# Kernel optimization log

Measured on AMD Instinct MI355X. Metric: run time of the kernel, lower is better.

## Reference

```python
import jax, jax.numpy as jnp
import numpy as np

N_LAYERS = 10
N_BLOCKS = 2
N_FILTERS = 2
N_CHANNELS = 1
KERNEL = 2
DIL_BASE = 2
N_RES = N_BLOCKS * N_LAYERS


def conv1d(x, w, b, dilation, pad):
    # x: [B, Cin, L], w: [Cout, Cin, K], b: [Cout]
    y = jax.lax.conv_general_dilated(
        x, w, window_strides=(1,), padding=[(pad, pad)],
        rhs_dilation=(dilation,), dimension_numbers=("NCH", "OIH", "NCH"))
    return y + b[None, :, None]


def setup_inputs() -> dict:
    key = jax.random.key(0)
    ks = jax.random.split(key, 9)
    B, C, L = 64, N_CHANNELS, 32768
    f = N_FILTERS
    s_in = 1.0 / np.sqrt(C * 1)          # conv_in fan-in (k=1)
    s_res = 1.0 / np.sqrt(f * KERNEL)    # residual conv fan-in
    s_out = 1.0 / np.sqrt(f * 1)         # conv_out fan-in (k=1)
    return {
        "x": jax.random.normal(ks[0], (B, C, L), dtype=jnp.float32),
        "conv_in_w": jax.random.normal(ks[1], (f, C, 1), dtype=jnp.float32) * s_in,
        "conv_in_b": jax.random.normal(ks[2], (f,), dtype=jnp.float32) * s_in,
        "wd": jax.random.normal(ks[3], (N_RES, f, f, KERNEL), dtype=jnp.float32) * s_res,
        "bd": jax.random.normal(ks[4], (N_RES, f), dtype=jnp.float32) * s_res,
        "wg": jax.random.normal(ks[5], (N_RES, f, f, KERNEL), dtype=jnp.float32) * s_res,
        "bg": jax.random.normal(ks[6], (N_RES, f), dtype=jnp.float32) * s_res,
        "conv_out_w": jax.random.normal(ks[7], (C, f, 1), dtype=jnp.float32) * s_out,
        "conv_out_b": jax.random.normal(ks[8], (C,), dtype=jnp.float32) * s_out,
    }


def reference(x, conv_in_w, conv_in_b, wd, bd, wg, bg, conv_out_w, conv_out_b):
    h = conv1d(x, conv_in_w, conv_in_b, 1, 0)  # [B, F, L]
    skips = []
    for i in range(N_RES):
        d = DIL_BASE ** (i // N_LAYERS)        # dilation constant within a block
        pad = (KERNEL - 1) * d // 2            # torch padding (padding arg is 0)
        cd = conv1d(h, wd[i], bd[i], d, pad)
        cg = conv1d(h, wg[i], bg[i], d, pad)
        g = cd * jax.nn.sigmoid(cg)            # gated activation (tanh unused in source)
        skips.append(g)
        # res = x[:, :, -g.size(2):] + g
        h = h[:, :, h.shape[2] - g.shape[2]:] + g
    # Faithful to torch: len(s) is the BATCH dim, so skips are truncated to time len B
    max_len = min(s.shape[0] for s in skips)
    s = skips[0][:, :, :max_len]
    for si in skips[1:]:
        s = s + si[:, :, :max_len]
    return conv1d(jax.nn.relu(s), conv_out_w, conv_out_b, 1, 0)
```

## Files before the change

kernel.cpp:

```cpp
#include <hip/hip_runtime.h>
#include <math.h>


#define N_RES   20
#define N_L1    10
#define W       96
#define OUT_L   64

__global__ __launch_bounds__(128) void wavenet_window_kernel(
    const float* __restrict__ x,
    const float* __restrict__ cin_w,
    const float* __restrict__ cin_b,
    const float* __restrict__ wd,
    const float* __restrict__ bd,
    const float* __restrict__ wg,
    const float* __restrict__ bg,
    const float* __restrict__ cout_w,
    const float* __restrict__ cout_b,
    float* __restrict__ out,
    int L)
{
    __shared__ float hbuf[2][2][W];
    __shared__ float skip[2][OUT_L];

    const int b   = blockIdx.x;
    const int tid = threadIdx.x;
    const float* xb = x + (size_t)b * (size_t)L;

    for (int idx = tid; idx < 2 * W; idx += blockDim.x) {
        const int f = idx / W, l = idx % W;
        hbuf[0][f][l] = cin_w[f] * xb[l] + cin_b[f];
    }
    for (int idx = tid; idx < 2 * OUT_L; idx += blockDim.x) {
        skip[idx / OUT_L][idx % OUT_L] = 0.0f;
    }
    __syncthreads();

    int cur = 0;
    int valid = W;
    for (int i = 0; i < N_RES; ++i) {
        const int d = (i < N_L1) ? 1 : 2;
        const float* wdi = wd + i * 8;
        const float* wgi = wg + i * 8;
        const float bd0 = bd[i * 2 + 0], bd1 = bd[i * 2 + 1];
        const float bg0 = bg[i * 2 + 0], bg1 = bg[i * 2 + 1];
        const int nout = valid - 1;

        for (int idx = tid; idx < 2 * W; idx += blockDim.x) {
            const int f = idx / W, l = idx % W;
            if (l < nout) {
                const int t0 = l - (d - 1);
                const float a0 = (t0 >= 0) ? hbuf[cur][0][t0] : 0.0f;
                const float a1 = (t0 >= 0) ? hbuf[cur][1][t0] : 0.0f;
                const float c0 = hbuf[cur][0][l + 1];
                const float c1 = hbuf[cur][1][l + 1];

                const float bdv = (f == 0) ? bd0 : bd1;
                const float bgv = (f == 0) ? bg0 : bg1;
                const float cd = wdi[f*4 + 0] * a0 + wdi[f*4 + 1] * c0
                               + wdi[f*4 + 2] * a1 + wdi[f*4 + 3] * c1 + bdv;
                const float cg = wgi[f*4 + 0] * a0 + wgi[f*4 + 1] * c0
                               + wgi[f*4 + 2] * a1 + wgi[f*4 + 3] * c1 + bgv;

                const float g = cd * (1.0f / (1.0f + expf(-cg)));
                const float hres = (d == 1) ? hbuf[cur][f][l + 1] : hbuf[cur][f][l];
                hbuf[1 - cur][f][l] = hres + g;
                if (l < OUT_L) skip[f][l] += g;
            }
        }
        __syncthreads();
        cur = 1 - cur;
        valid = nout;
    }

    const float w0 = cout_w[0], w1 = cout_w[1], bo = cout_b[0];
    for (int l = tid; l < OUT_L; l += blockDim.x) {
        const float s0 = fmaxf(skip[0][l], 0.0f);
        const float s1 = fmaxf(skip[1][l], 0.0f);
        out[(size_t)b * OUT_L + l] = w0 * s0 + w1 * s1 + bo;
    }
}

extern "C" void kernel_launch(void* const* d_in, const int* in_sizes, int n_in,
                              void* d_out, int out_size, void* d_ws, size_t ws_size,
                              hipStream_t stream) {
    const float* x      = (const float*)d_in[0];
    const float* cin_w  = (const float*)d_in[1];
    const float* cin_b  = (const float*)d_in[2];
    const float* wd     = (const float*)d_in[3];
    const float* bd     = (const float*)d_in[4];
    const float* wg     = (const float*)d_in[5];
    const float* bg     = (const float*)d_in[6];
    const float* cout_w = (const float*)d_in[7];
    const float* cout_b = (const float*)d_in[8];
    float* out = (float*)d_out;

    const int B = 64;
    const int L = in_sizes[0] / B;

    wavenet_window_kernel<<<B, 128, 0, stream>>>(
        x, cin_w, cin_b, wd, bd, wg, bg, cout_w, cout_b, out, L);
}
```

Measured before the change: 84.08 us.

## Remap to one wavefront per window computing both filters per lane

Shrinks each block to a single 64-lane wavefront, so each lane computes both output filters for its time position. This shares the four input loads from shared memory and removes the per-element filter branch. The 16 weights per layer are loaded once into scalars instead of being indexed per element, and expf is replaced with the faster, less precise __expf. With only one wavefront, __syncthreads becomes cheap, but the block has half as many threads to hide latency.

```diff
diff --git a/kernel.cpp b/kernel.cpp
--- a/kernel.cpp
+++ b/kernel.cpp
@@ -7,7 +7,7 @@
 #define W       96
 #define OUT_L   64
 
-__global__ __launch_bounds__(128) void wavenet_window_kernel(
+__global__ __launch_bounds__(64) void wavenet_window_kernel(
     const float* __restrict__ x,
     const float* __restrict__ cin_w,
     const float* __restrict__ cin_b,
@@ -23,16 +23,23 @@
     __shared__ float hbuf[2][2][W];
     __shared__ float skip[2][OUT_L];
 
-    const int b   = blockIdx.x;
-    const int tid = threadIdx.x;
+    const int b    = blockIdx.x;
+    const int lane = threadIdx.x;
     const float* xb = x + (size_t)b * (size_t)L;
 
-    for (int idx = tid; idx < 2 * W; idx += blockDim.x) {
-        const int f = idx / W, l = idx % W;
-        hbuf[0][f][l] = cin_w[f] * xb[l] + cin_b[f];
-    }
-    for (int idx = tid; idx < 2 * OUT_L; idx += blockDim.x) {
-        skip[idx / OUT_L][idx % OUT_L] = 0.0f;
+    {
+        const float cw0 = cin_w[0], cw1 = cin_w[1];
+        const float cb0 = cin_b[0], cb1 = cin_b[1];
+        const float xv = xb[lane];
+        hbuf[0][0][lane] = cw0 * xv + cb0;
+        hbuf[0][1][lane] = cw1 * xv + cb1;
+        if (lane < W - 64) {
+            const float xv2 = xb[lane + 64];
+            hbuf[0][0][lane + 64] = cw0 * xv2 + cb0;
+            hbuf[0][1][lane + 64] = cw1 * xv2 + cb1;
+        }
+        skip[0][lane] = 0.0f;
+        skip[1][lane] = 0.0f;
     }
     __syncthreads();
 
@@ -42,12 +49,17 @@
         const int d = (i < N_L1) ? 1 : 2;
         const float* wdi = wd + i * 8;
         const float* wgi = wg + i * 8;
+        const float wd00 = wdi[0], wd01 = wdi[1], wd02 = wdi[2], wd03 = wdi[3];
+        const float wd10 = wdi[4], wd11 = wdi[5], wd12 = wdi[6], wd13 = wdi[7];
+        const float wg00 = wgi[0], wg01 = wgi[1], wg02 = wgi[2], wg03 = wgi[3];
+        const float wg10 = wgi[4], wg11 = wgi[5], wg12 = wgi[6], wg13 = wgi[7];
         const float bd0 = bd[i * 2 + 0], bd1 = bd[i * 2 + 1];
         const float bg0 = bg[i * 2 + 0], bg1 = bg[i * 2 + 1];
         const int nout = valid - 1;
+        const int nxt  = 1 - cur;
 
-        for (int idx = tid; idx < 2 * W; idx += blockDim.x) {
-            const int f = idx / W, l = idx % W;
+        for (int l0 = 0; l0 < nout; l0 += 64) {
+            const int l = l0 + lane;
             if (l < nout) {
                 const int t0 = l - (d - 1);
                 const float a0 = (t0 >= 0) ? hbuf[cur][0][t0] : 0.0f;
@@ -55,30 +67,33 @@
                 const float c0 = hbuf[cur][0][l + 1];
                 const float c1 = hbuf[cur][1][l + 1];
 
-                const float bdv = (f == 0) ? bd0 : bd1;
-                const float bgv = (f == 0) ? bg0 : bg1;
-                const float cd = wdi[f*4 + 0] * a0 + wdi[f*4 + 1] * c0
-                               + wdi[f*4 + 2] * a1 + wdi[f*4 + 3] * c1 + bdv;
-                const float cg = wgi[f*4 + 0] * a0 + wgi[f*4 + 1] * c0
-                               + wgi[f*4 + 2] * a1 + wgi[f*4 + 3] * c1 + bgv;
+                const float cd_0 = wd00*a0 + wd01*c0 + wd02*a1 + wd03*c1 + bd0;
+                const float cg_0 = wg00*a0 + wg01*c0 + wg02*a1 + wg03*c1 + bg0;
+                const float cd_1 = wd10*a0 + wd11*c0 + wd12*a1 + wd13*c1 + bd1;
+                const float cg_1 = wg10*a0 + wg11*c0 + wg12*a1 + wg13*c1 + bg1;
 
-                const float g = cd * (1.0f / (1.0f + expf(-cg)));
-                const float hres = (d == 1) ? hbuf[cur][f][l + 1] : hbuf[cur][f][l];
-                hbuf[1 - cur][f][l] = hres + g;
-                if (l < OUT_L) skip[f][l] += g;
+                const float g0 = cd_0 * (1.0f / (1.0f + __expf(-cg_0)));
+                const float g1 = cd_1 * (1.0f / (1.0f + __expf(-cg_1)));
+
+                const float hr0 = (d == 1) ? hbuf[cur][0][l + 1] : hbuf[cur][0][l];
+                const float hr1 = (d == 1) ? hbuf[cur][1][l + 1] : hbuf[cur][1][l];
+                hbuf[nxt][0][l] = hr0 + g0;
+                hbuf[nxt][1][l] = hr1 + g1;
+                if (l < OUT_L) {
+                    skip[0][l] += g0;
+                    skip[1][l] += g1;
+                }
             }
         }
         __syncthreads();
-        cur = 1 - cur;
+        cur = nxt;
         valid = nout;
     }
 
     const float w0 = cout_w[0], w1 = cout_w[1], bo = cout_b[0];
-    for (int l = tid; l < OUT_L; l += blockDim.x) {
-        const float s0 = fmaxf(skip[0][l], 0.0f);
-        const float s1 = fmaxf(skip[1][l], 0.0f);
-        out[(size_t)b * OUT_L + l] = w0 * s0 + w1 * s1 + bo;
-    }
+    const float s0 = fmaxf(skip[0][lane], 0.0f);
+    const float s1 = fmaxf(skip[1][lane], 0.0f);
+    out[(size_t)b * OUT_L + lane] = w0 * s0 + w1 * s1 + bo;
 }
 
 extern "C" void kernel_launch(void* const* d_in, const int* in_sizes, int n_in,
@@ -98,6 +113,6 @@
     const int B = 64;
     const int L = in_sizes[0] / B;
 
-    wavenet_window_kernel<<<B, 128, 0, stream>>>(
+    wavenet_window_kernel<<<B, 64, 0, stream>>>(
         x, cin_w, cin_b, wd, bd, wg, bg, cout_w, cout_b, out, L);
 }
```

Result: no change. 84.07 us (-0.0%).
